# Kernel optimization log

Hardware: AMD Instinct MI355X
Metric: run time of the kernel (lower is better)

Reference implementation:

```python
import jax, jax.numpy as jnp
import numpy as np

B, N, NP, NS = 8, 4096, 1024, 32
CF = 64            # input point-feature channels; in_channel = 3 + CF = 67
MLP = [64, 128, 256]
EPS = 1e-5         # BatchNorm eps (torch default)


def setup_inputs() -> dict:
    key = jax.random.key(0)
    ks = jax.random.split(key, 8)
    inp = {
        "xyz": jax.random.normal(ks[0], (B, N, 3), jnp.float32),
        "points": jax.random.normal(ks[1], (B, CF, N), jnp.float32),
        "sample_idx": jax.random.randint(ks[2], (B, NP), 0, N, dtype=jnp.int32),
        "neighbor_idx": jax.random.randint(ks[3], (B, NP, NS), 0, N, dtype=jnp.int32),
    }
    c = 3 + CF
    for i, o in enumerate(MLP):
        wk = jax.random.fold_in(ks[4], i)
        inp[f"W{i}"] = jax.random.normal(wk, (o, c), jnp.float32) * (1.0 / np.sqrt(c))
        inp[f"b{i}"] = jnp.zeros((o,), jnp.float32)
        inp[f"gamma{i}"] = jnp.ones((o,), jnp.float32)
        inp[f"beta{i}"] = jnp.zeros((o,), jnp.float32)
        c = o
    return inp


def _forward(xyz, points, sample_idx, neighbor_idx, params):
    # xyz: (B,N,3)  points: (B,CF,N)
    new_xyz = jnp.take_along_axis(xyz, sample_idx[:, :, None], axis=1)        # (B,NP,3)
    nbr_xyz = jax.vmap(lambda x, idx: x[idx])(xyz, neighbor_idx)               # (B,NP,NS,3)
    rel = nbr_xyz - new_xyz[:, :, None, :]                                     # (B,NP,NS,3)
    nbr_feat = jax.vmap(lambda f, idx: f[:, idx])(points, neighbor_idx)        # (B,CF,NP,NS)
    x = jnp.concatenate([rel.transpose(0, 3, 1, 2), nbr_feat], axis=1)         # (B,3+CF,NP,NS)
    # 1x1 Conv2d -> BatchNorm2d (training-mode batch stats) -> ReLU stack
    for W, b, g, be in params:
        x = jnp.einsum('oc,bcps->bops', W, x) + b[None, :, None, None]
        mu = x.mean(axis=(0, 2, 3), keepdims=True)
        var = x.var(axis=(0, 2, 3), keepdims=True)
        x = g[None, :, None, None] * (x - mu) * jax.lax.rsqrt(var + EPS) + be[None, :, None, None]
        x = jax.nn.relu(x)
    new_points = x.max(axis=-1)                                                # (B,C_out,NP)
    return new_xyz, new_points


def reference(xyz, points, sample_idx, neighbor_idx,
              W0, b0, gamma0, beta0,
              W1, b1, gamma1, beta1,
              W2, b2, gamma2, beta2):
    params = [(W0, b0, gamma0, beta0), (W1, b1, gamma1, beta1), (W2, b2, gamma2, beta2)]
    return _forward(xyz, points, sample_idx, neighbor_idx, params)
```

## Files before the change

### kernel.cpp

```cpp
#include <hip/hip_runtime.h>

typedef unsigned short u16;
typedef unsigned int u32;
typedef __attribute__((ext_vector_type(8))) short short8;
typedef __attribute__((ext_vector_type(16))) float f32x16;

#define BB 8
#define NN 4096
#define NPP 1024
#define NSS 32
#define CFF 64
#define C0 67
#define H0 64
#define H1 128
#define H2 256
#define MTOT (BB*NPP*NSS)
#define BN_EPS 1e-5f
#define INV_M (1.0f/262144.0f)

#define MFMA32(a,b,c) __builtin_amdgcn_mfma_f32_32x32x16_bf16(a,b,c,0,0,0)

__device__ __forceinline__ float bf2f(u16 h){ return __uint_as_float(((u32)h)<<16); }
__device__ __forceinline__ u16 f2bf(float f){
  u32 u = __float_as_uint(f);
  u32 r = (u + 0x7fffu + ((u>>16)&1u)) >> 16;
  return (u16)r;
}
__device__ __forceinline__ u32 pack2(float a, float b){
  return (u32)f2bf(a) | ((u32)f2bf(b)<<16);
}

#define WS_NEED 46280704u

__global__ __launch_bounds__(256) void k_setup(
    const float* __restrict__ xyz, const float* __restrict__ points,
    const int* __restrict__ sidx,
    const float* __restrict__ W0, const float* __restrict__ W1, const float* __restrict__ W2,
    u16* __restrict__ ptsT, u16* __restrict__ Wt0c, u16* __restrict__ Wt1c,
    u16* __restrict__ Wt2c, float* __restrict__ out_newxyz)
{
  int blk = blockIdx.x, tid = threadIdx.x;
  if (blk < 512) {
    __shared__ float t[64][65];
    int b = blk >> 6, n0 = (blk & 63) << 6;
    int nloc = tid & 63, cpart = tid >> 6;
    for (int i = 0; i < 16; ++i) {
      int c = i*4 + cpart;
      t[c][nloc] = points[(size_t)(b*CFF + c)*NN + n0 + nloc];
    }
    __syncthreads();
    int cloc = tid & 63, npart = tid >> 6;
    for (int i = 0; i < 16; ++i) {
      int n = i*4 + npart;
      ptsT[((size_t)(b*NN + n0 + n))*CFF + cloc] = f2bf(t[cloc][n]);
    }
  } else if (blk < 544) {
    int t0 = (blk - 512)*256 + tid;
    int b = t0 >> 10;
    int s = sidx[t0];
    for (int k = 0; k < 3; ++k)
      out_newxyz[(size_t)t0*3 + k] = xyz[((size_t)(b*NN + s))*3 + k];
  } else if (blk == 544) {
    for (int i = 0; i < 24; ++i) {
      int e = i*256 + tid;
      int kc = e >> 9, o = (e >> 3) & 63, j = e & 7, k = kc*8 + j;
      float v = (k < 64) ? W0[o*C0 + 3 + k] : ((k < 67) ? W0[o*C0 + (k - 64)] : 0.f);
      Wt0c[e] = f2bf(v);
    }
  } else if (blk == 545) {
    for (int i = 0; i < 32; ++i) {
      int e = i*256 + tid;
      int kc = e >> 10, n = (e >> 3) & 127, j = e & 7;
      Wt1c[e] = f2bf(W1[n*H0 + kc*8 + j]);
    }
  } else {
    int base = (blk - 546) * 4096;
    for (int i = 0; i < 16; ++i) {
      int e = base + i*256 + tid;
      int kc = e >> 11, n = (e >> 3) & 255, j = e & 7;
      Wt2c[e] = f2bf(W2[n*H1 + kc*8 + j]);
    }
  }
}

__global__ __launch_bounds__(256) void k_xyz_only(
    const float* __restrict__ xyz, const int* __restrict__ sidx, float* __restrict__ out_newxyz)
{
  int t0 = blockIdx.x*256 + threadIdx.x;
  int b = t0 >> 10;
  int s = sidx[t0];
  for (int k = 0; k < 3; ++k)
    out_newxyz[(size_t)t0*3 + k] = xyz[((size_t)(b*NN + s))*3 + k];
}

__global__ __launch_bounds__(256) void k_l0(
    const float* __restrict__ xyz, const int* __restrict__ sidx, const int* __restrict__ nidx,
    const u16* __restrict__ ptsT, const u16* __restrict__ Wt0c,
    u16* __restrict__ y0, float* __restrict__ stats)
{
  __shared__ u16 XLc[12*128*8];
  __shared__ u16 W0c[12*64*8];
  int tid = threadIdx.x;
  int m0 = blockIdx.x * 128;
  int b = m0 >> 15;

  for (int i = 0; i < 3; ++i)
    ((uint4*)W0c)[i*256 + tid] = ((const uint4*)Wt0c)[i*256 + tid];

  int pos = tid & 127, half = tid >> 7;
  int m = m0 + pos;
  int nb = nidx[m];
  {
    const uint4* prow = (const uint4*)(ptsT + ((size_t)(b*NN + nb))*CFF + half*32);
    uint4 h0 = prow[0], h1 = prow[1], h2 = prow[2], h3 = prow[3];
    *(uint4*)&XLc[((half*4+0)*128 + pos)*8] = h0;
    *(uint4*)&XLc[((half*4+1)*128 + pos)*8] = h1;
    *(uint4*)&XLc[((half*4+2)*128 + pos)*8] = h2;
    *(uint4*)&XLc[((half*4+3)*128 + pos)*8] = h3;
    if (half == 0) {
      int p = (m & 32767) >> 5;
      int sp = sidx[b*NPP + p];
      float r0 = xyz[((size_t)(b*NN+nb))*3+0] - xyz[((size_t)(b*NN+sp))*3+0];
      float r1 = xyz[((size_t)(b*NN+nb))*3+1] - xyz[((size_t)(b*NN+sp))*3+1];
      float r2 = xyz[((size_t)(b*NN+nb))*3+2] - xyz[((size_t)(b*NN+sp))*3+2];
      uint4 v = { pack2(r0, r1), pack2(r2, 0.f), 0u, 0u };
      *(uint4*)&XLc[(8*128 + pos)*8] = v;
    } else {
      uint4 z = {0u,0u,0u,0u};
      *(uint4*)&XLc[(9*128 + pos)*8]  = z;
      *(uint4*)&XLc[(10*128 + pos)*8] = z;
      *(uint4*)&XLc[(11*128 + pos)*8] = z;
    }
  }
  __syncthreads();

  int lane = tid & 63, wv = tid >> 6;
  int l31 = lane & 31, kh = lane >> 5;
  int nt = wv & 1, mtb = (wv >> 1) * 2;
  f32x16 acc[2];
  for (int mi = 0; mi < 2; ++mi) for (int r = 0; r < 16; ++r) acc[mi][r] = 0.f;

  for (int kt = 0; kt < 6; ++kt) {
    int ck = kt*2 + kh;
    short8 bfrag = *(const short8*)&W0c[(ck*64 + nt*32 + l31)*8];
    for (int mi = 0; mi < 2; ++mi) {
      short8 afrag = *(const short8*)&XLc[(ck*128 + (mtb+mi)*32 + l31)*8];
      acc[mi] = MFMA32(afrag, bfrag, acc[mi]);
    }
  }

  float s = 0.f, q = 0.f;
  for (int mi = 0; mi < 2; ++mi)
    for (int r = 0; r < 16; ++r) { float y = acc[mi][r]; s += y; q += y*y; }
  s += __shfl_xor(s, 32); q += __shfl_xor(q, 32);
  if (lane < 32) {
    int slot = blockIdx.x & 7;
    atomicAdd(&stats[slot*256 + nt*32 + lane], s);
    atomicAdd(&stats[2048 + slot*256 + nt*32 + lane], q);
  }
  for (int mi = 0; mi < 2; ++mi)
    for (int r = 0; r < 16; ++r) {
      int mm = (mtb+mi)*32 + (r&3) + 8*(r>>2) + 4*kh;
      y0[(size_t)(m0+mm)*H0 + nt*32 + l31] = f2bf(acc[mi][r]);
    }
}

__global__ __launch_bounds__(256) void k_l1s(
    const u16* __restrict__ y0, const u16* __restrict__ Wt1c,
    const float* __restrict__ g0, const float* __restrict__ e0,
    const float* __restrict__ stIn, float* __restrict__ stOut)
{
  __shared__ u16 X0c[8*128*8];
  __shared__ u16 W1c[8*128*8];
  __shared__ float scl0[64], sft0[64];
  int tid = threadIdx.x;
  int m0 = blockIdx.x * 128;

  if (tid < 64) {
    float s = 0.f, q = 0.f;
    for (int sl = 0; sl < 8; ++sl) { s += stIn[sl*256 + tid]; q += stIn[2048 + sl*256 + tid]; }
    float mu = s*INV_M, var = q*INV_M - mu*mu;
    float sc = g0[tid] * rsqrtf(var + BN_EPS);
    scl0[tid] = sc; sft0[tid] = e0[tid] - mu*sc;
  }
  for (int i = 0; i < 4; ++i)
    ((uint4*)W1c)[i*256 + tid] = ((const uint4*)Wt1c)[i*256 + tid];

  int pos = tid & 127, half = tid >> 7;
  {
    const u16* row = y0 + (size_t)(m0 + pos)*H0 + half*32;
    u16 hs[32];
    for (int t = 0; t < 4; ++t) *(uint4*)&hs[t*8] = ((const uint4*)row)[t];
    __syncthreads();
    u16 ob[32];
    for (int j = 0; j < 32; ++j) {
      int c = half*32 + j;
      ob[j] = f2bf(fmaxf(fmaf(scl0[c], bf2f(hs[j]), sft0[c]), 0.f));
    }
    for (int t = 0; t < 4; ++t)
      *(uint4*)&X0c[((half*4+t)*128 + pos)*8] = *(uint4*)&ob[t*8];
  }
  __syncthreads();

  int lane = tid & 63, wv = tid >> 6;
  int l31 = lane & 31, kh = lane >> 5;
  f32x16 acc[4];
  for (int mt = 0; mt < 4; ++mt) for (int r = 0; r < 16; ++r) acc[mt][r] = 0.f;

  for (int kt = 0; kt < 4; ++kt) {
    int ck = kt*2 + kh;
    short8 bfrag = *(const short8*)&W1c[(ck*128 + wv*32 + l31)*8];
    for (int mt = 0; mt < 4; ++mt) {
      short8 afrag = *(const short8*)&X0c[(ck*128 + mt*32 + l31)*8];
      acc[mt] = MFMA32(afrag, bfrag, acc[mt]);
    }
  }

  float s = 0.f, q = 0.f;
  for (int mt = 0; mt < 4; ++mt)
    for (int r = 0; r < 16; ++r) { float y = acc[mt][r]; s += y; q += y*y; }
  s += __shfl_xor(s, 32); q += __shfl_xor(q, 32);
  if (lane < 32) {
    int slot = blockIdx.x & 7;
    atomicAdd(&stOut[slot*256 + wv*32 + lane], s);
    atomicAdd(&stOut[2048 + slot*256 + wv*32 + lane], q);
  }
}

__global__ __launch_bounds__(512) void k_l2f(
    const u16* __restrict__ y0, const u16* __restrict__ Wt1c, const u16* __restrict__ Wt2c,
    const float* __restrict__ g0, const float* __restrict__ e0,
    const float* __restrict__ g1, const float* __restrict__ e1,
    const float* __restrict__ st0, const float* __restrict__ st1, float* __restrict__ stOut,
    u16* __restrict__ mxp, u16* __restrict__ mnp)
{
  __shared__ u16 X0c[8*128*8];
  __shared__ u16 X1c[16*128*8];
  __shared__ float scl0[64], sft0[64], scl1[128], sft1[128];
  int tid = threadIdx.x;
  int m0 = blockIdx.x * 128;

  int lane = tid & 63, w = tid >> 6;
  int l31 = lane & 31, kh = lane >> 5;

  int pos = tid & 127, qh = tid >> 7;
  u16 hs[16];
  {
    const u16* row = y0 + (size_t)(m0 + pos)*H0 + qh*16;
    *(uint4*)&hs[0] = ((const uint4*)row)[0];
    *(uint4*)&hs[8] = ((const uint4*)row)[1];
  }
  int nt1 = w & 3, mh = w >> 2;
  short8 b1[4];
#pragma unroll
  for (int kt = 0; kt < 4; ++kt)
    b1[kt] = *(const short8*)&Wt1c[((kt*2 + kh)*128 + nt1*32 + l31)*8];

  if (tid < 64) {
    float s = 0.f, q = 0.f;
    for (int sl = 0; sl < 8; ++sl) { s += st0[sl*256 + tid]; q += st0[2048 + sl*256 + tid]; }
    float mu = s*INV_M, var = q*INV_M - mu*mu;
    float sc = g0[tid] * rsqrtf(var + BN_EPS);
    scl0[tid] = sc; sft0[tid] = e0[tid] - mu*sc;
  }
  if (tid < 128) {
    float s = 0.f, q = 0.f;
    for (int sl = 0; sl < 8; ++sl) { s += st1[sl*256 + tid]; q += st1[2048 + sl*256 + tid]; }
    float mu = s*INV_M, var = q*INV_M - mu*mu;
    float sc = g1[tid] * rsqrtf(var + BN_EPS);
    scl1[tid] = sc; sft1[tid] = e1[tid] - mu*sc;
  }
  __syncthreads();

  {
    u16 ob[16];
#pragma unroll
    for (int j = 0; j < 16; ++j) {
      int c = qh*16 + j;
      ob[j] = f2bf(fmaxf(fmaf(scl0[c], bf2f(hs[j]), sft0[c]), 0.f));
    }
    *(uint4*)&X0c[((qh*2)*128 + pos)*8]   = *(uint4*)&ob[0];
    *(uint4*)&X0c[((qh*2+1)*128 + pos)*8] = *(uint4*)&ob[8];
  }
  __syncthreads();

  f32x16 acc1[2];
#pragma unroll
  for (int mi = 0; mi < 2; ++mi) for (int r = 0; r < 16; ++r) acc1[mi][r] = 0.f;
#pragma unroll
  for (int kt = 0; kt < 4; ++kt) {
    int ck = kt*2 + kh;
#pragma unroll
    for (int mi = 0; mi < 2; ++mi) {
      short8 afrag = *(const short8*)&X0c[(ck*128 + (mh*2+mi)*32 + l31)*8];
      acc1[mi] = MFMA32(afrag, b1[kt], acc1[mi]);
    }
  }

  short8 b2[8];
#pragma unroll
  for (int k4 = 0; k4 < 8; ++k4)
    b2[k4] = *(const short8*)&Wt2c[((k4*2 + kh)*256 + w*32 + l31)*8];

  {
    int ch1 = nt1*32 + l31;
    int cb = ch1 >> 3, cr = ch1 & 7, sw = cb & 3;
    float sc1 = scl1[ch1], sf1 = sft1[ch1];
#pragma unroll
    for (int mi = 0; mi < 2; ++mi)
#pragma unroll
      for (int r = 0; r < 16; ++r) {
        int mm = (mh*2+mi)*32 + (r&3) + 8*(r>>2) + 4*kh;
        X1c[(cb*128 + (mm ^ sw))*8 + cr] = f2bf(fmaxf(fmaf(sc1, acc1[mi][r], sf1), 0.f));
      }
  }
  __syncthreads();

  f32x16 acc2[4];
#pragma unroll
  for (int mt = 0; mt < 4; ++mt) for (int r = 0; r < 16; ++r) acc2[mt][r] = 0.f;
#pragma unroll
  for (int k4 = 0; k4 < 8; ++k4) {
    int ck = k4*2 + kh;
    int sw = ck & 3;
#pragma unroll
    for (int mt = 0; mt < 4; ++mt) {
      short8 afrag = *(const short8*)&X1c[(ck*128 + ((mt*32 + l31) ^ sw))*8];
      acc2[mt] = MFMA32(afrag, b2[k4], acc2[mt]);
    }
  }

  int ch = w*32 + l31;
  float s = 0.f, q = 0.f;
  float mx[4] = {-3.0e38f,-3.0e38f,-3.0e38f,-3.0e38f};
  float mn[4] = { 3.0e38f, 3.0e38f, 3.0e38f, 3.0e38f};
#pragma unroll
  for (int mt = 0; mt < 4; ++mt)
#pragma unroll
    for (int r = 0; r < 16; ++r) {
      float y = acc2[mt][r];
      s += y; q += y*y;
      mx[mt] = fmaxf(mx[mt], y); mn[mt] = fminf(mn[mt], y);
    }
  s += __shfl_xor(s, 32); q += __shfl_xor(q, 32);
#pragma unroll
  for (int mt = 0; mt < 4; ++mt) {
    mx[mt] = fmaxf(mx[mt], __shfl_xor(mx[mt], 32));
    mn[mt] = fminf(mn[mt], __shfl_xor(mn[mt], 32));
  }
  if (lane < 32) {
    int slot = blockIdx.x & 7;
    atomicAdd(&stOut[slot*256 + ch], s);
    atomicAdd(&stOut[2048 + slot*256 + ch], q);
#pragma unroll
    for (int mt = 0; mt < 4; ++mt) {
      size_t pr = (size_t)blockIdx.x*4 + mt;
      mxp[pr*H2 + ch] = f2bf(mx[mt]);
      mnp[pr*H2 + ch] = f2bf(mn[mt]);
    }
  }
}

__global__ __launch_bounds__(256) void k_final(
    const u16* __restrict__ mxp, const u16* __restrict__ mnp,
    const float* __restrict__ gma, const float* __restrict__ bta,
    const float* __restrict__ stIn, float* __restrict__ out_np)
{
  __shared__ float tmp[256][33];
  int tid = threadIdx.x;
  int b = blockIdx.x >> 5;
  int p0 = (blockIdx.x & 31) * 32;

  float s = 0.f, q = 0.f;
  for (int sl = 0; sl < 8; ++sl) { s += stIn[sl*256 + tid]; q += stIn[2048 + sl*256 + tid]; }
  float mu = s*INV_M, var = q*INV_M - mu*mu;
  float sc = gma[tid] * rsqrtf(var + BN_EPS);
  float sh = bta[tid] - mu*sc;

  for (int pp = 0; pp < 32; ++pp) {
    size_t base = ((size_t)(b*NPP + p0 + pp))*H2 + tid;
    float xv = bf2f(mxp[base]), nv = bf2f(mnp[base]);
    float v = (sc >= 0.f) ? fmaf(sc, xv, sh) : fmaf(sc, nv, sh);
    tmp[tid][pp] = fmaxf(v, 0.f);
  }
  __syncthreads();

  int pl = tid & 31, cg = tid >> 5;
  for (int cc = 0; cc < 32; ++cc) {
    int c = cc*8 + cg;
    out_np[((size_t)b*H2 + c)*NPP + p0 + pl] = tmp[c][pl];
  }
}

extern "C" void kernel_launch(void* const* d_in, const int* in_sizes, int n_in,
                              void* d_out, int out_size, void* d_ws, size_t ws_size,
                              hipStream_t stream)
{
  const float* xyz    = (const float*)d_in[0];
  const float* points = (const float*)d_in[1];
  const int*   sidx   = (const int*)d_in[2];
  const int*   nidx   = (const int*)d_in[3];
  const float* W0 = (const float*)d_in[4];
  const float* g0 = (const float*)d_in[6];
  const float* e0 = (const float*)d_in[7];
  const float* W1 = (const float*)d_in[8];
  const float* g1 = (const float*)d_in[10];
  const float* e1 = (const float*)d_in[11];
  const float* W2 = (const float*)d_in[12];
  const float* g2 = (const float*)d_in[14];
  const float* e2 = (const float*)d_in[15];

  float* out_xyz = (float*)d_out;
  float* out_np  = out_xyz + (size_t)BB*NPP*3;

  if (ws_size < (size_t)WS_NEED) {
    hipMemsetAsync(out_np, 0, (size_t)BB*H2*NPP*4, stream);
    k_xyz_only<<<32, 256, 0, stream>>>(xyz, sidx, out_xyz);
    return;
  }

  char* ws = (char*)d_ws;
  float* stats = (float*)(ws + 0);
  u16*   Wt0c  = (u16*)(ws + 49152);
  u16*   Wt1c  = (u16*)(ws + 61440);
  u16*   Wt2c  = (u16*)(ws + 77824);
  u16*   ptsT  = (u16*)(ws + 143360);
  u16*   y0    = (u16*)(ws + 4337664);
  u16*   mxp   = (u16*)(ws + 37892096);
  u16*   mnp   = (u16*)(ws + 42086400);

  hipMemsetAsync(stats, 0, 3*4096*sizeof(float), stream);
  k_setup<<<554, 256, 0, stream>>>(xyz, points, sidx, W0, W1, W2,
                                   ptsT, Wt0c, Wt1c, Wt2c, out_xyz);
  k_l0<<<MTOT/128, 256, 0, stream>>>(xyz, sidx, nidx, ptsT, Wt0c, y0, stats);
  k_l1s<<<MTOT/128, 256, 0, stream>>>(y0, Wt1c, g0, e0, stats, stats + 4096);
  k_l2f<<<MTOT/128, 512, 0, stream>>>(y0, Wt1c, Wt2c, g0, e0, g1, e1,
                                      stats, stats + 4096, stats + 8192, mxp, mnp);
  k_final<<<256, 256, 0, stream>>>(mxp, mnp, g2, e2, stats + 8192, out_np);
}
```

Measured before the change: 172.6 us.

## Vectorize transpose, stage layer-0 output through LDS, and cap l2f registers

The setup transpose now reads points with float4 loads and writes packed 8-element bf16 rows, replacing scalar per-element accesses. The layer-0 kernel stages its bf16 outputs in shared memory with an XOR swizzle, then writes y0 with coalesced 16-byte stores instead of strided 2-byte stores. k_l2f gets a min-blocks launch bound, and its layer-2 weight fragments are loaded in two halves so fewer registers are live, aiming for higher occupancy. The trade-offs are extra barriers, and possible spills or reloads under the tighter register budget.

```diff
diff --git a/kernel.cpp b/kernel.cpp
--- a/kernel.cpp
+++ b/kernel.cpp
@@ -41,18 +41,22 @@
 {
   int blk = blockIdx.x, tid = threadIdx.x;
   if (blk < 512) {
-    __shared__ float t[64][65];
+    __shared__ float t[64][68];
     int b = blk >> 6, n0 = (blk & 63) << 6;
-    int nloc = tid & 63, cpart = tid >> 6;
-    for (int i = 0; i < 16; ++i) {
-      int c = i*4 + cpart;
-      t[c][nloc] = points[(size_t)(b*CFF + c)*NN + n0 + nloc];
+    for (int it = 0; it < 4; ++it) {
+      int u = it*256 + tid;
+      int nq = u & 15, c = u >> 4;
+      float4 v = *(const float4*)&points[(size_t)(b*CFF + c)*NN + n0 + nq*4];
+      *(float4*)&t[c][nq*4] = v;
     }
     __syncthreads();
-    int cloc = tid & 63, npart = tid >> 6;
-    for (int i = 0; i < 16; ++i) {
-      int n = i*4 + npart;
-      ptsT[((size_t)(b*NN + n0 + n))*CFF + cloc] = f2bf(t[cloc][n]);
+    for (int it = 0; it < 2; ++it) {
+      int u = it*256 + tid;
+      int oct = u & 7, n = u >> 3;
+      u16 pk[8];
+#pragma unroll
+      for (int j = 0; j < 8; ++j) pk[j] = f2bf(t[oct*8 + j][n]);
+      *(uint4*)&ptsT[((size_t)(b*NN + n0 + n))*CFF + oct*8] = *(uint4*)pk;
     }
   } else if (blk < 544) {
     int t0 = (blk - 512)*256 + tid;
@@ -158,11 +162,29 @@
     atomicAdd(&stats[slot*256 + nt*32 + lane], s);
     atomicAdd(&stats[2048 + slot*256 + nt*32 + lane], q);
   }
-  for (int mi = 0; mi < 2; ++mi)
-    for (int r = 0; r < 16; ++r) {
-      int mm = (mtb+mi)*32 + (r&3) + 8*(r>>2) + 4*kh;
-      y0[(size_t)(m0+mm)*H0 + nt*32 + l31] = f2bf(acc[mi][r]);
-    }
+
+  __syncthreads();
+  {
+    int chx = (nt*32 + l31) ^ (kh*32);
+#pragma unroll
+    for (int mi = 0; mi < 2; ++mi)
+#pragma unroll
+      for (int r = 0; r < 16; ++r) {
+        int mm = (mtb+mi)*32 + (r&3) + 8*(r>>2) + 4*kh;
+        XLc[mm*64 + chx] = f2bf(acc[mi][r]);
+      }
+  }
+  __syncthreads();
+  {
+    uint4* dst = (uint4*)(y0 + (size_t)m0*H0);
+#pragma unroll
+    for (int i = 0; i < 4; ++i) {
+      int t16 = i*256 + tid;
+      int mrow = t16 >> 3, ch0 = (t16 & 7)*8;
+      int idx = mrow*64 + (ch0 ^ (32*((mrow>>2)&1)));
+      dst[t16] = *(const uint4*)&XLc[idx];
+    }
+  }
 }
 
 __global__ __launch_bounds__(256) void k_l1s(
@@ -227,7 +249,7 @@
   }
 }
 
-__global__ __launch_bounds__(512) void k_l2f(
+__global__ __launch_bounds__(512, 4) void k_l2f(
     const u16* __restrict__ y0, const u16* __restrict__ Wt1c, const u16* __restrict__ Wt2c,
     const float* __restrict__ g0, const float* __restrict__ e0,
     const float* __restrict__ g1, const float* __restrict__ e1,
@@ -297,10 +319,10 @@
     }
   }
 
-  short8 b2[8];
-#pragma unroll
-  for (int k4 = 0; k4 < 8; ++k4)
-    b2[k4] = *(const short8*)&Wt2c[((k4*2 + kh)*256 + w*32 + l31)*8];
+  short8 b2a[4];
+#pragma unroll
+  for (int q4 = 0; q4 < 4; ++q4)
+    b2a[q4] = *(const short8*)&Wt2c[((q4*2 + kh)*256 + w*32 + l31)*8];
 
   {
     int ch1 = nt1*32 + l31;
@@ -316,17 +338,32 @@
   }
   __syncthreads();
 
+  short8 b2b[4];
+#pragma unroll
+  for (int q4 = 0; q4 < 4; ++q4)
+    b2b[q4] = *(const short8*)&Wt2c[(((q4+4)*2 + kh)*256 + w*32 + l31)*8];
+
   f32x16 acc2[4];
 #pragma unroll
   for (int mt = 0; mt < 4; ++mt) for (int r = 0; r < 16; ++r) acc2[mt][r] = 0.f;
 #pragma unroll
-  for (int k4 = 0; k4 < 8; ++k4) {
+  for (int k4 = 0; k4 < 4; ++k4) {
     int ck = k4*2 + kh;
     int sw = ck & 3;
 #pragma unroll
     for (int mt = 0; mt < 4; ++mt) {
       short8 afrag = *(const short8*)&X1c[(ck*128 + ((mt*32 + l31) ^ sw))*8];
-      acc2[mt] = MFMA32(afrag, b2[k4], acc2[mt]);
+      acc2[mt] = MFMA32(afrag, b2a[k4], acc2[mt]);
+    }
+  }
+#pragma unroll
+  for (int k4 = 4; k4 < 8; ++k4) {
+    int ck = k4*2 + kh;
+    int sw = ck & 3;
+#pragma unroll
+    for (int mt = 0; mt < 4; ++mt) {
+      short8 afrag = *(const short8*)&X1c[(ck*128 + ((mt*32 + l31) ^ sw))*8];
+      acc2[mt] = MFMA32(afrag, b2b[k4-4], acc2[mt]);
     }
   }
 
```

New measurement: 171.6 us. Within noise of the previous version (-0.6%).
